# Kernel optimization log

Hardware: AMD Instinct MI355X
Metric: run time of the kernel (lower is better)

The kernel has to match this reference:

```python
import jax, jax.numpy as jnp
import numpy as np

N, D = 8192, 1024

def setup_inputs() -> dict:
    key = jax.random.key(0)
    ks = jax.random.split(key, 7)
    s = 1.0 / np.sqrt(D)  # mimic nn.Linear init scale
    return {
        "embeddings": jax.random.normal(ks[0], (N, D), jnp.float32),
        "Wq": jax.random.normal(ks[1], (D, D), jnp.float32) * s,
        "bq": jax.random.normal(ks[2], (D,), jnp.float32) * s,
        "Wk": jax.random.normal(ks[3], (D, D), jnp.float32) * s,
        "bk": jax.random.normal(ks[4], (D,), jnp.float32) * s,
        "Wv": jax.random.normal(ks[5], (D, D), jnp.float32) * s,
        "bv": jax.random.normal(ks[6], (D,), jnp.float32) * s,
    }

def reference(embeddings, Wq, bq, Wk, bk, Wv, bv):
    # nn.Linear: y = x @ W^T + b; weights here are stored as [out, in] equivalent (square), use x @ W.T
    q = embeddings @ Wq.T + bq          # [N, D]
    k = embeddings @ Wk.T + bk          # [N, D]
    v = embeddings @ Wv.T + bv          # [N, D]
    scores = q @ k.T                    # [N, N]  (unscaled, as in source)
    attn = jax.nn.softmax(scores, axis=-1)
    out = attn @ v                      # [N, D]
    return out[:, None, :]              # [N, 1, D] matching torch broadcasted-matmul output
```

## Files before the change

kernel.cpp:

```cpp
#include <hip/hip_runtime.h>
#include <hip/hip_fp16.h>
#include <cstdint>
#include <cstddef>

typedef _Float16 half8 __attribute__((ext_vector_type(8)));
typedef _Float16 half4 __attribute__((ext_vector_type(4)));
typedef float floatx4 __attribute__((ext_vector_type(4)));
typedef float floatx16 __attribute__((ext_vector_type(16)));

#define N_TOK 8192
#define DIM   1024

#define EPI_F32   0
#define EPI_PART  1

#define FENCE_BARRIER() asm volatile("s_barrier" ::: "memory")
#define WAIT_VM4()      asm volatile("s_waitcnt vmcnt(4)" ::: "memory")
#define WAIT_VM0()      asm volatile("s_waitcnt vmcnt(0)" ::: "memory")

__device__ __forceinline__ void async_tile16(const _Float16* gp, _Float16* lp) {
    __builtin_amdgcn_global_load_lds(
        (const __attribute__((address_space(1))) void*)gp,
        (__attribute__((address_space(3))) void*)lp, 16, 0, 0);
}

template<int EPI, bool FOLD, bool REMAP>
__global__ __launch_bounds__(512)
void gemm8(const _Float16* __restrict__ Ahi, const _Float16* __restrict__ Alo,
           const _Float16* __restrict__ B, int lda, int ldb, int ntiles,
           float* __restrict__ C, int ldc)
{
    __shared__ _Float16 smem[65536];

    int bx = blockIdx.x, by = blockIdx.y, bz = blockIdx.z;
    if constexpr (REMAP) {
        const int gx = gridDim.x, gy = gridDim.y;
        const int gxy = gx * gy;
        const int nb = gxy * gridDim.z;
        const int bid = bz * gxy + by * gx + bx;
        const int nid = (bid & 7) * (nb >> 3) + (bid >> 3);
        bx = nid % gx; by = (nid / gx) % gy; bz = nid / gxy;
    }

    const int tid  = threadIdx.x;
    const int lane = tid & 63;
    const int w    = tid >> 6;
    const int wm   = w >> 2;
    const int wn   = w & 3;
    const int l15  = lane & 15;
    const int l4   = lane >> 4;
    const int row0 = by * 256;
    const int col0 = bx * 256;
    const int kbeg_t = FOLD ? 0 : bz * ntiles;

    const int r_s = tid >> 3;
    const int j_s = tid & 7;

    _Float16* A0 = smem;
    _Float16* B0 = smem + 16384;
    _Float16* A1 = smem + 32768;
    _Float16* B1 = smem + 49152;

    const int co0 = ((l4)     ^ (l15 >> 1)) << 3;
    const int co1 = ((4 + l4) ^ (l15 >> 1)) << 3;

    floatx4 acc[8][4];
#pragma unroll
    for (int mi = 0; mi < 8; mi++)
#pragma unroll
        for (int ni = 0; ni < 4; ni++)
#pragma unroll
            for (int e = 0; e < 4; e++) acc[mi][ni][e] = 0.f;

    half8 af[4][2], bf[4][2];

    auto asrc = [&](int kt) -> const _Float16* {
        int ktc = kt > ntiles - 1 ? ntiles - 1 : kt;
        if constexpr (FOLD) {
            const _Float16* base = (ktc < 16) ? Ahi : Alo;
            return base + (size_t)row0 * lda + (ktc & 15) * 64;
        } else {
            return Ahi + (size_t)row0 * lda + (size_t)(kbeg_t + ktc) * 64;
        }
    };
    auto bsrc = [&](int kt) -> const _Float16* {
        int ktc = kt > ntiles - 1 ? ntiles - 1 : kt;
        const int kk = FOLD ? (ktc & 15) : (kbeg_t + ktc);
        return B + (size_t)col0 * ldb + (size_t)kk * 64;
    };

    auto stage = [&](const _Float16* tile, int ld, int half, _Float16* reg) {
#pragma unroll
        for (int p = 0; p < 2; p++) {
            const int r  = half * 128 + p * 64 + r_s;
            const int jg = j_s ^ ((r >> 1) & 7);
            async_tile16(tile + (size_t)r * ld + jg * 8, reg + r * 64 + j_s * 8);
        }
    };

    auto lda4 = [&](const _Float16* Ab, int mbase) {
#pragma unroll
        for (int m2 = 0; m2 < 4; m2++) {
            const int r = (wm * 128 + (mbase + m2) * 16 + l15) * 64;
            af[m2][0] = *(const half8*)&Ab[r + co0];
            af[m2][1] = *(const half8*)&Ab[r + co1];
        }
    };
    auto ldb2 = [&](const _Float16* Bb, int nbase) {
#pragma unroll
        for (int n2 = 0; n2 < 2; n2++) {
            const int r = (wn * 64 + (nbase + n2) * 16 + l15) * 64;
            bf[nbase + n2][0] = *(const half8*)&Bb[r + co0];
            bf[nbase + n2][1] = *(const half8*)&Bb[r + co1];
        }
    };
    auto quad = [&](int qm, int qn) {
        __builtin_amdgcn_s_setprio(1);
#pragma unroll
        for (int m2 = 0; m2 < 4; m2++)
#pragma unroll
            for (int n2 = 0; n2 < 2; n2++)
#pragma unroll
                for (int kk = 0; kk < 2; kk++)
                    acc[qm * 4 + m2][qn * 2 + n2] =
                        __builtin_amdgcn_mfma_f32_16x16x32_f16(
                            af[m2][kk], bf[qn * 2 + n2][kk],
                            acc[qm * 4 + m2][qn * 2 + n2], 0, 0, 0);
        __builtin_amdgcn_s_setprio(0);
    };

    stage(bsrc(0), ldb, 0, B0); stage(bsrc(0), ldb, 1, B0);
    stage(asrc(0), lda, 0, A0); stage(asrc(0), lda, 1, A0);
    stage(bsrc(1), ldb, 0, B1); stage(bsrc(1), ldb, 1, B1);
    WAIT_VM4();
    FENCE_BARRIER();

    const int NIc = ntiles >> 1;
    for (int i = 0; i < NIc; i++) {
        const int t1 = 2 * i + 1, t2 = 2 * i + 2, t3 = 2 * i + 3;
        ldb2(B0, 0); lda4(A0, 0); stage(asrc(t1), lda, 0, A1);
        FENCE_BARRIER(); quad(0, 0); FENCE_BARRIER();
        ldb2(B0, 2); stage(asrc(t1), lda, 1, A1);
        FENCE_BARRIER(); quad(0, 1); FENCE_BARRIER();
        lda4(A0, 4); stage(bsrc(t2), ldb, 0, B0);
        FENCE_BARRIER(); quad(1, 0); FENCE_BARRIER();
        stage(bsrc(t2), ldb, 1, B0);
        FENCE_BARRIER(); quad(1, 1); WAIT_VM4(); FENCE_BARRIER();
        ldb2(B1, 0); lda4(A1, 0); stage(asrc(t2), lda, 0, A0);
        FENCE_BARRIER(); quad(0, 0); FENCE_BARRIER();
        ldb2(B1, 2); stage(asrc(t2), lda, 1, A0);
        FENCE_BARRIER(); quad(0, 1); FENCE_BARRIER();
        lda4(A1, 4); stage(bsrc(t3), ldb, 0, B1);
        FENCE_BARRIER(); quad(1, 0); FENCE_BARRIER();
        stage(bsrc(t3), ldb, 1, B1);
        FENCE_BARRIER(); quad(1, 1); WAIT_VM4(); FENCE_BARRIER();
    }
    WAIT_VM0();

#pragma unroll
    for (int mi = 0; mi < 8; mi++) {
#pragma unroll
        for (int ni = 0; ni < 4; ni++) {
            const int row = row0 + wm * 128 + mi * 16 + l4 * 4;
            const int col = col0 + wn * 64 + ni * 16 + l15;
#pragma unroll
            for (int r2 = 0; r2 < 4; r2++) {
                const float v = acc[mi][ni][r2];
                if constexpr (EPI == EPI_F32) {
                    C[(size_t)(row + r2) * ldc + col] = v;
                } else {
                    C[(size_t)(row + r2) * ldc + (size_t)bz * DIM + col] = v;
                }
            }
        }
    }
}

template<int BM, int BN, int BK>
__global__ __launch_bounds__(256)
void gemm_qkv(const _Float16* __restrict__ Ehi, const _Float16* __restrict__ Elo,
              const _Float16* __restrict__ W,
              _Float16* __restrict__ qhi, _Float16* __restrict__ qlo,
              _Float16* __restrict__ khi, _Float16* __restrict__ vtr,
              const float* __restrict__ bq, const float* __restrict__ bk,
              const float* __restrict__ bv)
{
    constexpr int MI = BM / 64;
    constexpr int NI = BN / 64;
    constexpr int CPR = BK / 8;
    constexpr int SW  = CPR - 1;
    constexpr int RPP = 2048 / BK;
    constexpr int IA  = BM * BK / 2048;
    constexpr int IB  = BN * BK / 2048;
    constexpr int A_ELTS = BM * BK;
    constexpr int B_ELTS = BN * BK;
    __shared__ _Float16 smem[2 * A_ELTS + B_ELTS];
    constexpr int tAhi = 0;
    constexpr int tAlo = A_ELTS;
    constexpr int tB   = 2 * A_ELTS;

    int bx = blockIdx.x, by = blockIdx.y, bz = blockIdx.z;
    {
        const int gx = gridDim.x, gy = gridDim.y;
        const int gxy = gx * gy;
        const int nb = gxy * gridDim.z;
        const int bid = bz * gxy + by * gx + bx;
        const int nid = (bid & 7) * (nb >> 3) + (bid >> 3);
        bx = nid % gx; by = (nid / gx) % gy; bz = nid / gxy;
    }
    const int unit = bz;
    const bool dolo = (unit < 2);

    const int tid  = threadIdx.x;
    const int row0 = by * BM;
    const int col0 = bx * BN;
    const int lane = tid & 63;
    const int w    = tid >> 6;
    const int wm   = w & 1, wn = w >> 1;
    const int l31  = lane & 31, lhi = lane >> 5;

    floatx16 acc[MI][NI];
#pragma unroll
    for (int mi = 0; mi < MI; mi++)
#pragma unroll
        for (int ni = 0; ni < NI; ni++)
#pragma unroll
            for (int e = 0; e < 16; e++) acc[mi][ni][e] = 0.f;

    const int r_s = tid / CPR;
    const int j_s = tid % CPR;
    const size_t brow0 = (size_t)(unit * DIM + col0);

    for (int k0 = 0; k0 < DIM; k0 += BK) {
        __syncthreads();
#pragma unroll
        for (int i = 0; i < IA; i++) {
            const int r = i * RPP + r_s;
            const int jg = j_s ^ ((r >> 1) & SW);
            async_tile16(Ehi + (size_t)(row0 + r) * DIM + k0 + jg * 8,
                         smem + tAhi + (i * 256 + tid) * 8);
            if (dolo)
                async_tile16(Elo + (size_t)(row0 + r) * DIM + k0 + jg * 8,
                             smem + tAlo + (i * 256 + tid) * 8);
        }
#pragma unroll
        for (int i = 0; i < IB; i++) {
            const int r = i * RPP + r_s;
            const int jg = j_s ^ ((r >> 1) & SW);
            async_tile16(W + (brow0 + r) * DIM + k0 + jg * 8,
                         smem + tB + (i * 256 + tid) * 8);
        }
        __syncthreads();

#pragma unroll
        for (int ks = 0; ks < BK / 16; ks++) {
            half8 af[MI], bf[NI], al[MI];
            const int cb = ks * 2 + lhi;
#pragma unroll
            for (int mi = 0; mi < MI; mi++) {
                const int r = wm * (BM / 2) + mi * 32 + l31;
                const int cj = (cb ^ ((r >> 1) & SW)) * 8;
                af[mi] = *(half8*)&smem[tAhi + r * BK + cj];
                if (dolo) al[mi] = *(half8*)&smem[tAlo + r * BK + cj];
            }
#pragma unroll
            for (int ni = 0; ni < NI; ni++) {
                const int r = wn * (BN / 2) + ni * 32 + l31;
                const int cj = (cb ^ ((r >> 1) & SW)) * 8;
                bf[ni] = *(half8*)&smem[tB + r * BK + cj];
            }
#pragma unroll
            for (int mi = 0; mi < MI; mi++)
#pragma unroll
                for (int ni = 0; ni < NI; ni++)
                    acc[mi][ni] = __builtin_amdgcn_mfma_f32_32x32x16_f16(af[mi], bf[ni], acc[mi][ni], 0, 0, 0);
            if (dolo) {
#pragma unroll
                for (int mi = 0; mi < MI; mi++)
#pragma unroll
                    for (int ni = 0; ni < NI; ni++)
                        acc[mi][ni] = __builtin_amdgcn_mfma_f32_32x32x16_f16(al[mi], bf[ni], acc[mi][ni], 0, 0, 0);
            }
        }
    }

    const float* bias = (unit == 0) ? bq : (unit == 1) ? bk : bv;
#pragma unroll
    for (int mi = 0; mi < MI; mi++) {
#pragma unroll
        for (int ni = 0; ni < NI; ni++) {
            const int colg = col0 + wn * (BN / 2) + ni * 32 + l31;
            const float bb = bias[colg];
            const int base = row0 + wm * (BM / 2) + mi * 32 + 4 * lhi;
#pragma unroll
            for (int g = 0; g < 4; g++) {
                const int rowb = base + 8 * g;
                if (unit == 2) {
                    half4 hv;
#pragma unroll
                    for (int r2 = 0; r2 < 4; r2++) hv[r2] = (_Float16)(acc[mi][ni][4 * g + r2] + bb);
                    *(half4*)&vtr[(size_t)colg * N_TOK + rowb] = hv;
                } else {
#pragma unroll
                    for (int r2 = 0; r2 < 4; r2++) {
                        const int rowg = rowb + r2;
                        const float t = acc[mi][ni][4 * g + r2] + bb;
                        const _Float16 hi = (_Float16)t;
                        if (unit == 0) {
                            qhi[(size_t)rowg * DIM + colg] = hi;
                            qlo[(size_t)rowg * DIM + colg] = (_Float16)(t - (float)hi);
                        } else {
                            khi[(size_t)rowg * DIM + colg] = hi;
                        }
                    }
                }
            }
        }
    }
}

__global__ __launch_bounds__(256)
void split_inputs(const float* __restrict__ E,
                  const float* __restrict__ Wq, const float* __restrict__ Wk, const float* __restrict__ Wv,
                  _Float16* __restrict__ Ehi, _Float16* __restrict__ Elo,
                  _Float16* __restrict__ Wqh, _Float16* __restrict__ Wkh, _Float16* __restrict__ Wvh)
{
    const int u = blockIdx.y;
    const size_t idx = ((size_t)blockIdx.x * 256 + threadIdx.x) * 4;
    const size_t MM = (size_t)DIM * DIM;
    const float* src; _Float16* dhi; _Float16* dlo = nullptr;
    if (u < 8)      { src = E + u * MM;  dhi = Ehi + u * MM; dlo = Elo + u * MM; }
    else if (u == 8){ src = Wq; dhi = Wqh; }
    else if (u == 9){ src = Wk; dhi = Wkh; }
    else            { src = Wv; dhi = Wvh; }
    const float4 f = *(const float4*)(src + idx);
    half4 hh;
    hh[0] = (_Float16)f.x; hh[1] = (_Float16)f.y; hh[2] = (_Float16)f.z; hh[3] = (_Float16)f.w;
    *(half4*)(dhi + idx) = hh;
    if (u < 8) {
        half4 hl;
        hl[0] = (_Float16)(f.x - (float)hh[0]); hl[1] = (_Float16)(f.y - (float)hh[1]);
        hl[2] = (_Float16)(f.z - (float)hh[2]); hl[3] = (_Float16)(f.w - (float)hh[3]);
        *(half4*)(dlo + idx) = hl;
    }
}

__global__ __launch_bounds__(256)
void softmax_rows(float* __restrict__ S, float* __restrict__ inv_l)
{
    __shared__ float srow[N_TOK];
    __shared__ float red[4];
    const int tid = threadIdx.x;
    float* row = S + (size_t)blockIdx.x * N_TOK;

    float mx = -3.0e38f;
#pragma unroll
    for (int i = 0; i < 8; i++) {
        const int v = i * 256 + tid;
        const float4 f = ((const float4*)row)[v];
        ((float4*)srow)[v] = f;
        mx = fmaxf(mx, fmaxf(fmaxf(f.x, f.y), fmaxf(f.z, f.w)));
    }
#pragma unroll
    for (int off = 32; off > 0; off >>= 1) mx = fmaxf(mx, __shfl_down(mx, off));
    if ((tid & 63) == 0) red[tid >> 6] = mx;
    __syncthreads();
    mx = fmaxf(fmaxf(red[0], red[1]), fmaxf(red[2], red[3]));
    __syncthreads();

    float sum = 0.f;
    _Float16* prow = (_Float16*)row;
#pragma unroll
    for (int i = 0; i < 8; i++) {
        const int v = i * 256 + tid;
        const float4 f = ((const float4*)srow)[v];
        const float e0 = __expf(f.x - mx), e1 = __expf(f.y - mx);
        const float e2 = __expf(f.z - mx), e3 = __expf(f.w - mx);
        sum += (e0 + e1) + (e2 + e3);
        half4 h; h[0] = (_Float16)e0; h[1] = (_Float16)e1; h[2] = (_Float16)e2; h[3] = (_Float16)e3;
        ((half4*)prow)[v] = h;
    }
#pragma unroll
    for (int off = 32; off > 0; off >>= 1) sum += __shfl_down(sum, off);
    if ((tid & 63) == 0) red[tid >> 6] = sum;
    __syncthreads();
    if (tid == 0) inv_l[blockIdx.x] = 1.f / (red[0] + red[1] + red[2] + red[3]);
}

__global__ __launch_bounds__(256)
void reduce_pv(const float* __restrict__ Sc, const float* __restrict__ invl,
               float* __restrict__ out)
{
    const int r  = blockIdx.x;
    const int c4 = threadIdx.x;
    const float* p = Sc + (size_t)r * N_TOK + N_TOK / 2 + (size_t)c4 * 4;
    float4 s = *(const float4*)p;
#pragma unroll
    for (int z = 1; z < 4; z++) {
        const float4 t = *(const float4*)(p + (size_t)z * DIM);
        s.x += t.x; s.y += t.y; s.z += t.z; s.w += t.w;
    }
    const float iv = invl[r];
    float4 o; o.x = s.x * iv; o.y = s.y * iv; o.z = s.z * iv; o.w = s.w * iv;
    *(float4*)(out + (size_t)r * DIM + (size_t)c4 * 4) = o;
}

extern "C" void kernel_launch(void* const* d_in, const int* in_sizes, int n_in,
                              void* d_out, int out_size, void* d_ws, size_t ws_size,
                              hipStream_t stream)
{
    const float* E  = (const float*)d_in[0];
    const float* Wq = (const float*)d_in[1];
    const float* bq = (const float*)d_in[2];
    const float* Wk = (const float*)d_in[3];
    const float* bk = (const float*)d_in[4];
    const float* Wv = (const float*)d_in[5];
    const float* bv = (const float*)d_in[6];
    float* out = (float*)d_out;

    char* ws = (char*)d_ws;
    const size_t SZ = (size_t)N_TOK * DIM * sizeof(_Float16);
    const size_t WW = (size_t)DIM * DIM * sizeof(_Float16);
    _Float16* q_hi = (_Float16*)(ws);
    _Float16* q_lo = (_Float16*)(ws + SZ);
    _Float16* k_hi = (_Float16*)(ws + 2 * SZ);
    _Float16* vt   = (_Float16*)(ws + 3 * SZ);
    float*    invl = (float*)(ws + 4 * SZ);
    char*     scratch = ws + 4 * SZ + 65536;
    _Float16* Ehi = (_Float16*)(scratch);
    _Float16* Elo = (_Float16*)(scratch + SZ);
    _Float16* Wqh = (_Float16*)(scratch + 2 * SZ);
    _Float16* Wkh = (_Float16*)(scratch + 2 * SZ + WW);
    _Float16* Wvh = (_Float16*)(scratch + 2 * SZ + 2 * WW);
    float*    Sc  = (float*)(scratch);
    const size_t esplit_bytes = 2 * SZ + 3 * WW;
    const size_t base = 4 * SZ + 65536;

    int NC = 256;
    const int cands[6] = {8192, 4096, 2048, 1024, 512, 256};
    for (int i = 0; i < 6; i++) {
        size_t sc = (size_t)cands[i] * N_TOK * 4;
        size_t need = base + (sc > esplit_bytes ? sc : esplit_bytes);
        if (ws_size >= need) { NC = cands[i]; break; }
    }

    const dim3 blk(256, 1, 1);
    const dim3 blk512(512, 1, 1);
    constexpr int KS = 4;

    split_inputs<<<dim3(DIM * DIM / 1024, 11, 1), blk, 0, stream>>>(
        E, Wq, Wk, Wv, Ehi, Elo, Wqh, Wkh, Wvh);

    gemm_qkv<128, 128, 64><<<dim3(DIM / 128, N_TOK / 128, 3), blk, 0, stream>>>(
        Ehi, Elo, Wqh, q_hi, q_lo, k_hi, vt, bq, bk, bv);

    const int nchunks = N_TOK / NC;
    for (int c = 0; c < nchunks; c++) {
        const size_t roff = (size_t)c * NC;
        gemm8<EPI_F32, true, true><<<dim3(N_TOK / 256, NC / 256, 1), blk512, 0, stream>>>(
            q_hi + roff * DIM, q_lo + roff * DIM, k_hi, DIM, DIM, 32, Sc, N_TOK);
        softmax_rows<<<dim3(NC, 1, 1), blk, 0, stream>>>(Sc, invl + roff);
        gemm8<EPI_PART, false, true><<<dim3(DIM / 256, NC / 256, KS), blk512, 0, stream>>>(
            (const _Float16*)Sc, nullptr, vt, 2 * N_TOK, N_TOK, 32, Sc + N_TOK / 2, N_TOK);
        reduce_pv<<<dim3(NC, 1, 1), blk, 0, stream>>>(Sc, invl + roff, out + roff * DIM);
    }
}
```

Measured before the change: 680.2 us.

## Double-buffer A fragments and overlap LDS reads with MFMA quads

Splits the A register fragments into two sets so LDS reads for the next quad are issued before the current quad's MFMAs. Explicit lgkmcnt waits and sched barriers let those reads overlap the matrix ops. It also precomputes the swizzled staging column once per thread. This adds register pressure and hand-counted wait counts, which could stall or be wrong if the counts are off.

```diff
diff --git a/kernel.cpp b/kernel.cpp
--- a/kernel.cpp
+++ b/kernel.cpp
@@ -17,6 +17,8 @@
 #define FENCE_BARRIER() asm volatile("s_barrier" ::: "memory")
 #define WAIT_VM4()      asm volatile("s_waitcnt vmcnt(4)" ::: "memory")
 #define WAIT_VM0()      asm volatile("s_waitcnt vmcnt(0)" ::: "memory")
+#define WAIT_LGKM(n)    asm volatile("s_waitcnt lgkmcnt(" #n ")" ::: "memory")
+#define SCHED0()        __builtin_amdgcn_sched_barrier(0)
 
 __device__ __forceinline__ void async_tile16(const _Float16* gp, _Float16* lp) {
     __builtin_amdgcn_global_load_lds(
@@ -53,8 +55,9 @@
     const int col0 = bx * 256;
     const int kbeg_t = FOLD ? 0 : bz * ntiles;
 
-    const int r_s = tid >> 3;
-    const int j_s = tid & 7;
+    const int r_s  = tid >> 3;
+    const int j_s  = tid & 7;
+    const int jcol = (j_s ^ ((r_s >> 1) & 7)) * 8;
 
     _Float16* A0 = smem;
     _Float16* B0 = smem + 16384;
@@ -72,7 +75,7 @@
 #pragma unroll
             for (int e = 0; e < 4; e++) acc[mi][ni][e] = 0.f;
 
-    half8 af[4][2], bf[4][2];
+    half8 af1[4][2], af2[4][2], bf[4][2];
 
     auto asrc = [&](int kt) -> const _Float16* {
         int ktc = kt > ntiles - 1 ? ntiles - 1 : kt;
@@ -89,24 +92,23 @@
         return B + (size_t)col0 * ldb + (size_t)kk * 64;
     };
 
-    auto stage = [&](const _Float16* tile, int ld, int half, _Float16* reg) {
+    auto stage = [&](const _Float16* tile, int ld, int half, _Float16* dst) {
 #pragma unroll
         for (int p = 0; p < 2; p++) {
-            const int r  = half * 128 + p * 64 + r_s;
-            const int jg = j_s ^ ((r >> 1) & 7);
-            async_tile16(tile + (size_t)r * ld + jg * 8, reg + r * 64 + j_s * 8);
-        }
-    };
-
-    auto lda4 = [&](const _Float16* Ab, int mbase) {
+            const int r = half * 128 + p * 64 + r_s;
+            async_tile16(tile + r * ld + jcol, dst + r * 64 + j_s * 8);
+        }
+    };
+
+    auto ldsA = [&](const _Float16* Ab, int mbase, half8 (*dst)[2]) {
 #pragma unroll
         for (int m2 = 0; m2 < 4; m2++) {
             const int r = (wm * 128 + (mbase + m2) * 16 + l15) * 64;
-            af[m2][0] = *(const half8*)&Ab[r + co0];
-            af[m2][1] = *(const half8*)&Ab[r + co1];
-        }
-    };
-    auto ldb2 = [&](const _Float16* Bb, int nbase) {
+            dst[m2][0] = *(const half8*)&Ab[r + co0];
+            dst[m2][1] = *(const half8*)&Ab[r + co1];
+        }
+    };
+    auto ldsB = [&](const _Float16* Bb, int nbase) {
 #pragma unroll
         for (int n2 = 0; n2 < 2; n2++) {
             const int r = (wn * 64 + (nbase + n2) * 16 + l15) * 64;
@@ -114,7 +116,7 @@
             bf[nbase + n2][1] = *(const half8*)&Bb[r + co1];
         }
     };
-    auto quad = [&](int qm, int qn) {
+    auto quad = [&](half8 (*A)[2], int qm, int qn) {
         __builtin_amdgcn_s_setprio(1);
 #pragma unroll
         for (int m2 = 0; m2 < 4; m2++)
@@ -124,7 +126,7 @@
                 for (int kk = 0; kk < 2; kk++)
                     acc[qm * 4 + m2][qn * 2 + n2] =
                         __builtin_amdgcn_mfma_f32_16x16x32_f16(
-                            af[m2][kk], bf[qn * 2 + n2][kk],
+                            A[m2][kk], bf[qn * 2 + n2][kk],
                             acc[qm * 4 + m2][qn * 2 + n2], 0, 0, 0);
         __builtin_amdgcn_s_setprio(0);
     };
@@ -134,26 +136,53 @@
     stage(bsrc(1), ldb, 0, B1); stage(bsrc(1), ldb, 1, B1);
     WAIT_VM4();
     FENCE_BARRIER();
+    ldsB(B0, 0); ldsA(A0, 0, af1);
 
     const int NIc = ntiles >> 1;
     for (int i = 0; i < NIc; i++) {
         const int t1 = 2 * i + 1, t2 = 2 * i + 2, t3 = 2 * i + 3;
-        ldb2(B0, 0); lda4(A0, 0); stage(asrc(t1), lda, 0, A1);
-        FENCE_BARRIER(); quad(0, 0); FENCE_BARRIER();
-        ldb2(B0, 2); stage(asrc(t1), lda, 1, A1);
-        FENCE_BARRIER(); quad(0, 1); FENCE_BARRIER();
-        lda4(A0, 4); stage(bsrc(t2), ldb, 0, B0);
-        FENCE_BARRIER(); quad(1, 0); FENCE_BARRIER();
+        stage(asrc(t1), lda, 0, A1);
+        ldsB(B0, 2);
+        FENCE_BARRIER(); WAIT_LGKM(4); SCHED0();
+        quad(af1, 0, 0);
+        FENCE_BARRIER();
+        stage(asrc(t1), lda, 1, A1);
+        ldsA(A0, 4, af2);
+        FENCE_BARRIER(); WAIT_LGKM(8); SCHED0();
+        quad(af1, 0, 1);
+        FENCE_BARRIER();
+        stage(bsrc(t2), ldb, 0, B0);
+        FENCE_BARRIER(); WAIT_LGKM(0); SCHED0();
+        quad(af2, 1, 0);
+        FENCE_BARRIER();
         stage(bsrc(t2), ldb, 1, B0);
-        FENCE_BARRIER(); quad(1, 1); WAIT_VM4(); FENCE_BARRIER();
-        ldb2(B1, 0); lda4(A1, 0); stage(asrc(t2), lda, 0, A0);
-        FENCE_BARRIER(); quad(0, 0); FENCE_BARRIER();
-        ldb2(B1, 2); stage(asrc(t2), lda, 1, A0);
-        FENCE_BARRIER(); quad(0, 1); FENCE_BARRIER();
-        lda4(A1, 4); stage(bsrc(t3), ldb, 0, B1);
-        FENCE_BARRIER(); quad(1, 0); FENCE_BARRIER();
+        WAIT_VM4();
+        FENCE_BARRIER();
+        ldsB(B1, 0); ldsA(A1, 0, af1);
+        WAIT_LGKM(12); SCHED0();
+        quad(af2, 1, 1);
+        FENCE_BARRIER();
+        stage(asrc(t2), lda, 0, A0);
+        ldsB(B1, 2);
+        FENCE_BARRIER(); WAIT_LGKM(4); SCHED0();
+        quad(af1, 0, 0);
+        FENCE_BARRIER();
+        stage(asrc(t2), lda, 1, A0);
+        ldsA(A1, 4, af2);
+        FENCE_BARRIER(); WAIT_LGKM(8); SCHED0();
+        quad(af1, 0, 1);
+        FENCE_BARRIER();
+        stage(bsrc(t3), ldb, 0, B1);
+        FENCE_BARRIER(); WAIT_LGKM(0); SCHED0();
+        quad(af2, 1, 0);
+        FENCE_BARRIER();
         stage(bsrc(t3), ldb, 1, B1);
-        FENCE_BARRIER(); quad(1, 1); WAIT_VM4(); FENCE_BARRIER();
+        WAIT_VM4();
+        FENCE_BARRIER();
+        ldsB(B0, 0); ldsA(A0, 0, af1);
+        WAIT_LGKM(12); SCHED0();
+        quad(af2, 1, 1);
+        FENCE_BARRIER();
     }
     WAIT_VM0();
 
```

New measurement: 1.066 ms. 1.57x slower.
